# Kernel tuning notes

Measured on AMD Instinct MI355X. Metric: run time of the kernel, lower is better.

## Reference

```python
import jax, jax.numpy as jnp
import numpy as np

D_MODEL, D_INT, H = 1024, 64, 16
LAMBDA_INIT = 0.8
B, S = 2, 2048
LN_EPS = 1e-5


def setup_inputs() -> dict:
    key = jax.random.key(0)
    ks = jax.random.split(key, 12)
    sd = 0.02
    return {
        "x": jax.random.normal(ks[0], (B, S, D_MODEL), dtype=jnp.float32),
        "lambda_current": jnp.float32(0.5),
        "mask": jnp.ones((B, S), dtype=jnp.int32),
        # stacked per-head params (WQ1/WK1/WV; WQ2/WK2 are unused in source due to bug)
        "wq": sd * jax.random.normal(ks[1], (H, D_MODEL, D_INT), dtype=jnp.float32),
        "bq": sd * jax.random.normal(ks[2], (H, D_INT), dtype=jnp.float32),
        "wk": sd * jax.random.normal(ks[3], (H, D_MODEL, D_INT), dtype=jnp.float32),
        "bk": sd * jax.random.normal(ks[4], (H, D_INT), dtype=jnp.float32),
        "wv": sd * jax.random.normal(ks[5], (H, D_MODEL, 2 * D_INT), dtype=jnp.float32),
        "bv": sd * jax.random.normal(ks[6], (H, 2 * D_INT), dtype=jnp.float32),
        "wo": sd * jax.random.normal(ks[7], (2 * H * D_INT, D_MODEL), dtype=jnp.float32),
        "bo": sd * jax.random.normal(ks[8], (D_MODEL,), dtype=jnp.float32),
        "ln_g": jnp.ones((2 * D_INT,), dtype=jnp.float32),
        "ln_b": jnp.zeros((2 * D_INT,), dtype=jnp.float32),
    }


def reference(x, lambda_current, mask, wq, bq, wk, bk, wv, bv, wo, bo, ln_g, ln_b):
    b, s, d_model = x.shape
    scale = 1.0 / (d_model ** 0.5)  # source divides by sqrt(WQ1.in_features)
    # per-head projections: [H, B, S, d]
    Q = jnp.einsum('bsd,hdk->hbsk', x, wq) + bq[:, None, None, :]
    K = jnp.einsum('bsd,hdk->hbsk', x, wk) + bk[:, None, None, :]
    V = jnp.einsum('bsd,hdv->hbsv', x, wv) + bv[:, None, None, :]
    scores = jnp.einsum('hbsk,hbtk->hbst', Q, K) * scale
    scores = jnp.where(mask[None, :, None, :] == 0, -jnp.inf, scores)
    A1 = jax.nn.softmax(scores, axis=-1)
    # source bug: Q2/K2 reuse WQ1/WK1 => A2 == A1, so A = A1 - lambda*A2 = (1-lambda)*A1
    A = (1.0 - lambda_current) * A1
    out = jnp.einsum('hbst,hbtv->hbsv', A, V)  # [H,B,S,2*D_INT]
    # per-head LayerNorm (shared gamma/beta), then scale by (1 - lambda_init)
    mu = out.mean(-1, keepdims=True)
    var = out.var(-1, keepdims=True)
    out = (out - mu) / jnp.sqrt(var + LN_EPS) * ln_g + ln_b
    out = out * (1.0 - LAMBDA_INIT)
    cat = out.transpose(1, 2, 0, 3).reshape(b, s, -1)  # concat heads on feature dim
    res = cat @ wo + bo
    return (res, A)
```

## Files before the change

kernel.cpp:

```cpp
#include <hip/hip_runtime.h>
#include <hip/hip_bf16.h>

#define DM   1024
#define DI   64
#define H_   16
#define B_   2
#define S_   2048
#define NTOK 4096

typedef unsigned short u16;
typedef __attribute__((ext_vector_type(8))) short s16x8;
typedef __attribute__((ext_vector_type(4))) float f32x4;
typedef __attribute__((ext_vector_type(4))) unsigned int u32x4;
typedef __attribute__((ext_vector_type(4))) unsigned short u16x4;

static __device__ __forceinline__ u16 f2bf(float f) {
  unsigned int u = __builtin_bit_cast(unsigned int, f);
  unsigned int r = (u + 0x7fffu + ((u >> 16) & 1u)) >> 16;
  return (u16)r;
}


__global__ void k_cvt_x(const float* __restrict__ in, u16* __restrict__ out) {
  int i = (blockIdx.x * 256 + threadIdx.x) * 4;
  float4 v = *(const float4*)&in[i];
  u16x4 o;
  o[0] = f2bf(v.x); o[1] = f2bf(v.y); o[2] = f2bf(v.z); o[3] = f2bf(v.w);
  *(u16x4*)&out[i] = o;
}

__global__ void k_small(const float* __restrict__ bq, const float* __restrict__ bk,
                        const float* __restrict__ bv, const int* __restrict__ mask,
                        float* __restrict__ bc, float* __restrict__ mbias) {
  int t = blockIdx.x * 256 + threadIdx.x;
  if (t < 1024) bc[t] = bq[t];
  else if (t < 2048) bc[t] = bk[t - 1024];
  else if (t < 4096) bc[t] = bv[t - 2048];
  else if (t < 8192) { int i = t - 4096; mbias[i] = mask[i] ? 0.f : -1e38f; }
}

__global__ void k_tr_f2b(const float* __restrict__ in, u16* __restrict__ out, int R, int C) {
  __shared__ float t[32][33];
  const float* src = in + (size_t)blockIdx.z * R * C;
  u16* dst = out + (size_t)blockIdx.z * C * R;
  int r0 = blockIdx.y * 32, c0 = blockIdx.x * 32;
  for (int i = threadIdx.y; i < 32; i += 8)
    t[i][threadIdx.x] = src[(size_t)(r0 + i) * C + c0 + threadIdx.x];
  __syncthreads();
  for (int i = threadIdx.y; i < 32; i += 8)
    dst[(size_t)(c0 + i) * R + r0 + threadIdx.x] = f2bf(t[threadIdx.x][i]);
}

__global__ void k_tr_b2b(const u16* __restrict__ in, u16* __restrict__ out, int R, int C) {
  __shared__ u16 t[32][33];
  const u16* src = in + (size_t)blockIdx.z * R * C;
  u16* dst = out + (size_t)blockIdx.z * C * R;
  int r0 = blockIdx.y * 32, c0 = blockIdx.x * 32;
  for (int i = threadIdx.y; i < 32; i += 8)
    t[i][threadIdx.x] = src[(size_t)(r0 + i) * C + c0 + threadIdx.x];
  __syncthreads();
  for (int i = threadIdx.y; i < 32; i += 8)
    dst[(size_t)(c0 + i) * R + r0 + threadIdx.x] = t[threadIdx.x][i];
}

template<int MODE>
__global__ __launch_bounds__(256)
void k_gemm(const u16* __restrict__ A, const u16* __restrict__ Bt,
            const float* __restrict__ bias, int Kdim,
            u16* __restrict__ q_out, u16* __restrict__ k_out, u16* __restrict__ v_out,
            float* __restrict__ res_out) {
  const int tid = threadIdx.x;
  const int l = tid & 63, w = tid >> 6;
  const int wm = w >> 1, wn = w & 1;
  const int g = l >> 4, lo = l & 15;
  const int m0 = blockIdx.y * 128, n0 = blockIdx.x * 128;
  __shared__ u16 As[128 * 72];
  __shared__ u16 Bs[128 * 72];
  f32x4 acc[4][4] = {};
  for (int kt = 0; kt < Kdim; kt += 64) {
    __syncthreads();
    for (int cid = tid; cid < 1024; cid += 256) {
      int r = cid >> 3, c = (cid & 7) * 8;
      *(u32x4*)&As[r * 72 + c] = *(const u32x4*)&A[(size_t)(m0 + r) * Kdim + kt + c];
      *(u32x4*)&Bs[r * 72 + c] = *(const u32x4*)&Bt[(size_t)(n0 + r) * Kdim + kt + c];
    }
    __syncthreads();
    for (int kc = 0; kc < 64; kc += 32) {
      s16x8 a[4], b[4];
      for (int i = 0; i < 4; i++)
        a[i] = *(const s16x8*)&As[(wm * 64 + i * 16 + lo) * 72 + kc + 8 * g];
      for (int i = 0; i < 4; i++)
        b[i] = *(const s16x8*)&Bs[(wn * 64 + i * 16 + lo) * 72 + kc + 8 * g];
      for (int mi = 0; mi < 4; mi++)
        for (int ni = 0; ni < 4; ni++)
          acc[mi][ni] = __builtin_amdgcn_mfma_f32_16x16x32_bf16(a[mi], b[ni], acc[mi][ni], 0, 0, 0);
    }
  }
  for (int mi = 0; mi < 4; mi++)
    for (int ni = 0; ni < 4; ni++)
      for (int j = 0; j < 4; j++) {
        int m = m0 + wm * 64 + mi * 16 + g * 4 + j;
        int n = n0 + wn * 64 + ni * 16 + lo;
        float v = acc[mi][ni][j] + bias[n];
        if (MODE == 0) {
          int bb = m >> 11, s = m & 2047;
          if (n < 1024) {
            int h = n >> 6, d = n & 63;
            q_out[(((size_t)h * B_ + bb) * S_ + s) * 64 + d] = f2bf(v);
          } else if (n < 2048) {
            int nn = n - 1024; int h = nn >> 6, d = nn & 63;
            k_out[(((size_t)h * B_ + bb) * S_ + s) * 64 + d] = f2bf(v);
          } else {
            int nn = n - 2048; int h = nn >> 7, d = nn & 127;
            v_out[(((size_t)h * B_ + bb) * S_ + s) * 128 + d] = f2bf(v);
          }
        } else {
          res_out[(size_t)m * 1024 + n] = v;
        }
      }
}

__global__ __launch_bounds__(512)
void k_attn(const u16* __restrict__ Qb, const u16* __restrict__ Kb,
            const u16* __restrict__ Vtb, const float* __restrict__ mbias,
            const float* __restrict__ lam_p, const float* __restrict__ ln_g,
            const float* __restrict__ ln_b, float* __restrict__ A_out,
            u16* __restrict__ cat) {
  const int tid = threadIdx.x, l = tid & 63, w = tid >> 6;
  const int g = l >> 4, lo = l & 15;
  const int bid = blockIdx.x;
  const int xcd = bid & 7, idx = bid >> 3;
  const int hb = xcd * 4 + (idx >> 4);
  const int s0 = (idx & 15) * 128;
  const int b = hb & 1, h = hb >> 1;
  const float scale2 = 0.03125f * 1.44269504f;

  __shared__ u16 Ks[2][64 * 72];
  __shared__ u16 Vs[2][128 * 72];
  __shared__ u16 Ps[8][16 * 72];

  const u16* Qhb = Qb + (size_t)hb * S_ * 64;
  const u16* Khb = Kb + (size_t)hb * S_ * 64;
  const u16* Vthb = Vtb + (size_t)hb * 128 * S_;
  const float* mb = mbias + (size_t)b * S_;

  const int kr = tid >> 3, kc8 = (tid & 7) * 8;

  const int q = s0 + w * 16 + lo;
  const s16x8 q0 = *(const s16x8*)&Qhb[(size_t)q * 64 + 8 * g];
  const s16x8 q1 = *(const s16x8*)&Qhb[(size_t)q * 64 + 32 + 8 * g];

  {
    u32x4 kreg = *(const u32x4*)&Khb[(size_t)kr * 64 + kc8];
    *(u32x4*)&Ks[0][kr * 72 + kc8] = kreg;
  }
  __syncthreads();
  float ps = 0.f;
  for (int t = 0; t < 32; t++) {
    const int kt = t * 64, buf = t & 1;
    const int ktn = (kt + 64) & (S_ - 1);
    u32x4 kreg = *(const u32x4*)&Khb[(size_t)(ktn + kr) * 64 + kc8];
#pragma unroll
    for (int nf = 0; nf < 4; nf++) {
      s16x8 k0 = *(const s16x8*)&Ks[buf][(nf * 16 + lo) * 72 + 8 * g];
      s16x8 k1 = *(const s16x8*)&Ks[buf][(nf * 16 + lo) * 72 + 32 + 8 * g];
      f32x4 z = {};
      z = __builtin_amdgcn_mfma_f32_16x16x32_bf16(k0, q0, z, 0, 0, 0);
      z = __builtin_amdgcn_mfma_f32_16x16x32_bf16(k1, q1, z, 0, 0, 0);
      f32x4 m4 = *(const f32x4*)&mb[kt + nf * 16 + g * 4];
      ps += __builtin_exp2f(z[0] * scale2 + m4[0]);
      ps += __builtin_exp2f(z[1] * scale2 + m4[1]);
      ps += __builtin_exp2f(z[2] * scale2 + m4[2]);
      ps += __builtin_exp2f(z[3] * scale2 + m4[3]);
    }
    *(u32x4*)&Ks[buf ^ 1][kr * 72 + kc8] = kreg;
    __syncthreads();
  }
  ps += __shfl_xor(ps, 16, 64);
  ps += __shfl_xor(ps, 32, 64);
  const float rinv = (1.0f - lam_p[0]) / ps;

  {
    u32x4 v0 = *(const u32x4*)&Vthb[(size_t)(tid >> 2) * S_ + ((tid & 3) * 8 + 0)];
  }
  {
#pragma unroll
    for (int i = 0; i < 2; i++) {
      int c2 = tid + i * 512;
      int r = c2 >> 3, ch = (c2 & 7) * 8;
      *(u32x4*)&Vs[0][r * 72 + ch] = *(const u32x4*)&Vthb[(size_t)r * S_ + ch];
    }
  }
  __syncthreads();

  f32x4 o[8] = {};
  for (int t = 0; t < 32; t++) {
    const int kt = t * 64, buf = t & 1;
    u32x4 kreg;
    u32x4 vreg0, vreg1;
    const bool pre = (t < 31);
    if (pre) {
      const int ktn = kt + 64;
      kreg = *(const u32x4*)&Khb[(size_t)(ktn + kr) * 64 + kc8];
      int c2a = tid, c2b = tid + 512;
      vreg0 = *(const u32x4*)&Vthb[(size_t)(c2a >> 3) * S_ + ktn + (c2a & 7) * 8];
      vreg1 = *(const u32x4*)&Vthb[(size_t)(c2b >> 3) * S_ + ktn + (c2b & 7) * 8];
    }
#pragma unroll
    for (int nf = 0; nf < 4; nf++) {
      s16x8 k0 = *(const s16x8*)&Ks[buf][(nf * 16 + lo) * 72 + 8 * g];
      s16x8 k1 = *(const s16x8*)&Ks[buf][(nf * 16 + lo) * 72 + 32 + 8 * g];
      f32x4 z = {};
      z = __builtin_amdgcn_mfma_f32_16x16x32_bf16(k0, q0, z, 0, 0, 0);
      z = __builtin_amdgcn_mfma_f32_16x16x32_bf16(k1, q1, z, 0, 0, 0);
      f32x4 m4 = *(const f32x4*)&mb[kt + nf * 16 + g * 4];
      f32x4 p4;
      p4[0] = __builtin_exp2f(z[0] * scale2 + m4[0]) * rinv;
      p4[1] = __builtin_exp2f(z[1] * scale2 + m4[1]) * rinv;
      p4[2] = __builtin_exp2f(z[2] * scale2 + m4[2]) * rinv;
      p4[3] = __builtin_exp2f(z[3] * scale2 + m4[3]) * rinv;
      __builtin_nontemporal_store(
          p4, (f32x4*)&A_out[((size_t)hb * S_ + q) * S_ + kt + nf * 16 + g * 4]);
      u16x4 pb;
      pb[0] = f2bf(p4[0]); pb[1] = f2bf(p4[1]);
      pb[2] = f2bf(p4[2]); pb[3] = f2bf(p4[3]);
      *(u16x4*)&Ps[w][lo * 72 + nf * 16 + g * 4] = pb;
    }
#pragma unroll
    for (int kc = 0; kc < 2; kc++) {
      s16x8 pa = *(const s16x8*)&Ps[w][lo * 72 + kc * 32 + 8 * g];
#pragma unroll
      for (int vf = 0; vf < 8; vf++) {
        s16x8 bv = *(const s16x8*)&Vs[buf][(vf * 16 + lo) * 72 + kc * 32 + 8 * g];
        o[vf] = __builtin_amdgcn_mfma_f32_16x16x32_bf16(pa, bv, o[vf], 0, 0, 0);
      }
    }
    if (pre) {
      *(u32x4*)&Ks[buf ^ 1][kr * 72 + kc8] = kreg;
      int c2a = tid, c2b = tid + 512;
      *(u32x4*)&Vs[buf ^ 1][(c2a >> 3) * 72 + (c2a & 7) * 8] = vreg0;
      *(u32x4*)&Vs[buf ^ 1][(c2b >> 3) * 72 + (c2b & 7) * 8] = vreg1;
    }
    __syncthreads();
  }

#pragma unroll
  for (int j = 0; j < 4; j++) {
    float sum = 0.f, sq = 0.f;
#pragma unroll
    for (int vf = 0; vf < 8; vf++) { float xv = o[vf][j]; sum += xv; sq += xv * xv; }
    for (int msk = 1; msk < 16; msk <<= 1) {
      sum += __shfl_xor(sum, msk, 64);
      sq += __shfl_xor(sq, msk, 64);
    }
    float mean = sum * (1.f / 128.f);
    float var = sq * (1.f / 128.f) - mean * mean;
    float rstd = rsqrtf(var + 1e-5f);
    int s = s0 + w * 16 + g * 4 + j;
    u16* cp = cat + ((size_t)(b * S_ + s)) * 2048 + h * 128;
#pragma unroll
    for (int vf = 0; vf < 8; vf++) {
      int c = vf * 16 + lo;
      float y = (o[vf][j] - mean) * rstd * ln_g[c] + ln_b[c];
      cp[c] = f2bf(y * 0.2f);
    }
  }
}


extern "C" void kernel_launch(void* const* d_in, const int* in_sizes, int n_in,
                              void* d_out, int out_size, void* d_ws, size_t ws_size,
                              hipStream_t stream) {
  const float* x    = (const float*)d_in[0];
  const float* lam  = (const float*)d_in[1];
  const int*   mask = (const int*)d_in[2];
  const float* wq   = (const float*)d_in[3];
  const float* bq   = (const float*)d_in[4];
  const float* wk   = (const float*)d_in[5];
  const float* bk   = (const float*)d_in[6];
  const float* wv   = (const float*)d_in[7];
  const float* bv   = (const float*)d_in[8];
  const float* wo   = (const float*)d_in[9];
  const float* bo   = (const float*)d_in[10];
  const float* lng  = (const float*)d_in[11];
  const float* lnb  = (const float*)d_in[12];

  float* res = (float*)d_out;
  float* A   = res + (size_t)NTOK * DM;

  char* ws = (char*)d_ws;
  size_t off = 0;
  auto alloc = [&](size_t bytes) {
    void* p = ws + off;
    off += (bytes + 255) & ~(size_t)255;
    return p;
  };
  u16*   xb    = (u16*)  alloc((size_t)NTOK * DM * 2);
  u16*   Wct   = (u16*)  alloc((size_t)4096 * 1024 * 2);
  float* bc    = (float*)alloc(4096 * 4);
  float* mbias = (float*)alloc(4096 * 4);
  u16*   wot   = (u16*)  alloc((size_t)1024 * 2048 * 2);
  u16*   Qb    = (u16*)  alloc((size_t)32 * S_ * 64 * 2);
  u16*   Kb2   = (u16*)  alloc((size_t)32 * S_ * 64 * 2);
  u16*   Vb    = (u16*)  alloc((size_t)32 * S_ * 128 * 2);
  u16*   Vtb   = (u16*)  alloc((size_t)32 * S_ * 128 * 2);
  u16*   catb  = (u16*)ws;

  k_cvt_x<<<4096, 256, 0, stream>>>(x, xb);
  k_small<<<32, 256, 0, stream>>>(bq, bk, bv, mask, bc, mbias);
  k_tr_f2b<<<dim3(2, 32, 16), dim3(32, 8), 0, stream>>>(wq, Wct, 1024, 64);
  k_tr_f2b<<<dim3(2, 32, 16), dim3(32, 8), 0, stream>>>(wk, Wct + 1024 * 1024, 1024, 64);
  k_tr_f2b<<<dim3(4, 32, 16), dim3(32, 8), 0, stream>>>(wv, Wct + 2048 * 1024, 1024, 128);
  k_tr_f2b<<<dim3(32, 64, 1), dim3(32, 8), 0, stream>>>(wo, wot, 2048, 1024);
  k_gemm<0><<<dim3(32, 32), 256, 0, stream>>>(xb, Wct, bc, 1024, Qb, Kb2, Vb, nullptr);
  k_tr_b2b<<<dim3(4, 64, 32), dim3(32, 8), 0, stream>>>(Vb, Vtb, 2048, 128);
  k_attn<<<dim3(512), 512, 0, stream>>>(Qb, Kb2, Vtb, mbias, lam, lng, lnb, A, catb);
  k_gemm<1><<<dim3(8, 32), 256, 0, stream>>>(catb, wot, bo, 2048, nullptr, nullptr, nullptr, res);
}
```

Measured before the change: 400.3 us.

## Process two query tiles per attention wave and use direct global-to-LDS loads in GEMM

The attention kernel now runs 4 waves of 256 threads, each owning 32 query rows split into two 16-row halves. Each K and V fragment read from LDS is reused for twice as many MFMAs, while staging loads per thread double. Separately, the GEMM replaces register-staged LDS fills with global_load_lds 16-byte direct loads into an unpadded 64-wide tile. That layout may add LDS bank conflicts on the fragment reads, and the attention kernel uses more registers with fewer waves per block.

```diff
diff --git a/kernel.cpp b/kernel.cpp
--- a/kernel.cpp
+++ b/kernel.cpp
@@ -9,15 +9,24 @@
 #define NTOK 4096
 
 typedef unsigned short u16;
+typedef unsigned int u32;
 typedef __attribute__((ext_vector_type(8))) short s16x8;
 typedef __attribute__((ext_vector_type(4))) float f32x4;
 typedef __attribute__((ext_vector_type(4))) unsigned int u32x4;
 typedef __attribute__((ext_vector_type(4))) unsigned short u16x4;
 
+#define AS1 __attribute__((address_space(1)))
+#define AS3 __attribute__((address_space(3)))
+
 static __device__ __forceinline__ u16 f2bf(float f) {
   unsigned int u = __builtin_bit_cast(unsigned int, f);
   unsigned int r = (u + 0x7fffu + ((u >> 16) & 1u)) >> 16;
   return (u16)r;
+}
+
+static __device__ __forceinline__ void gload_lds16(const u16* g, u16* l) {
+  __builtin_amdgcn_global_load_lds((const AS1 u32*)(const void*)g,
+                                   (AS3 u32*)(void*)l, 16, 0, 0);
 }
 
 
@@ -74,23 +83,23 @@
   const int wm = w >> 1, wn = w & 1;
   const int g = l >> 4, lo = l & 15;
   const int m0 = blockIdx.y * 128, n0 = blockIdx.x * 128;
-  __shared__ u16 As[128 * 72];
-  __shared__ u16 Bs[128 * 72];
+  __shared__ u16 As[128 * 64];
+  __shared__ u16 Bs[128 * 64];
   f32x4 acc[4][4] = {};
   for (int kt = 0; kt < Kdim; kt += 64) {
     __syncthreads();
     for (int cid = tid; cid < 1024; cid += 256) {
       int r = cid >> 3, c = (cid & 7) * 8;
-      *(u32x4*)&As[r * 72 + c] = *(const u32x4*)&A[(size_t)(m0 + r) * Kdim + kt + c];
-      *(u32x4*)&Bs[r * 72 + c] = *(const u32x4*)&Bt[(size_t)(n0 + r) * Kdim + kt + c];
+      gload_lds16(&A[(size_t)(m0 + r) * Kdim + kt + c], &As[cid * 8]);
+      gload_lds16(&Bt[(size_t)(n0 + r) * Kdim + kt + c], &Bs[cid * 8]);
     }
     __syncthreads();
     for (int kc = 0; kc < 64; kc += 32) {
       s16x8 a[4], b[4];
       for (int i = 0; i < 4; i++)
-        a[i] = *(const s16x8*)&As[(wm * 64 + i * 16 + lo) * 72 + kc + 8 * g];
+        a[i] = *(const s16x8*)&As[(wm * 64 + i * 16 + lo) * 64 + kc + 8 * g];
       for (int i = 0; i < 4; i++)
-        b[i] = *(const s16x8*)&Bs[(wn * 64 + i * 16 + lo) * 72 + kc + 8 * g];
+        b[i] = *(const s16x8*)&Bs[(wn * 64 + i * 16 + lo) * 64 + kc + 8 * g];
       for (int mi = 0; mi < 4; mi++)
         for (int ni = 0; ni < 4; ni++)
           acc[mi][ni] = __builtin_amdgcn_mfma_f32_16x16x32_bf16(a[mi], b[ni], acc[mi][ni], 0, 0, 0);
@@ -120,7 +129,7 @@
       }
 }
 
-__global__ __launch_bounds__(512)
+__global__ __launch_bounds__(256)
 void k_attn(const u16* __restrict__ Qb, const u16* __restrict__ Kb,
             const u16* __restrict__ Vtb, const float* __restrict__ mbias,
             const float* __restrict__ lam_p, const float* __restrict__ ln_g,
@@ -137,132 +146,174 @@
 
   __shared__ u16 Ks[2][64 * 72];
   __shared__ u16 Vs[2][128 * 72];
-  __shared__ u16 Ps[8][16 * 72];
+  __shared__ u16 Ps[4][32 * 72];
 
   const u16* Qhb = Qb + (size_t)hb * S_ * 64;
   const u16* Khb = Kb + (size_t)hb * S_ * 64;
   const u16* Vthb = Vtb + (size_t)hb * 128 * S_;
   const float* mb = mbias + (size_t)b * S_;
 
-  const int kr = tid >> 3, kc8 = (tid & 7) * 8;
-
-  const int q = s0 + w * 16 + lo;
-  const s16x8 q0 = *(const s16x8*)&Qhb[(size_t)q * 64 + 8 * g];
-  const s16x8 q1 = *(const s16x8*)&Qhb[(size_t)q * 64 + 32 + 8 * g];
+  s16x8 q0[2], q1[2];
+#pragma unroll
+  for (int qh = 0; qh < 2; qh++) {
+    const int q = s0 + w * 32 + qh * 16 + lo;
+    q0[qh] = *(const s16x8*)&Qhb[(size_t)q * 64 + 8 * g];
+    q1[qh] = *(const s16x8*)&Qhb[(size_t)q * 64 + 32 + 8 * g];
+  }
 
   {
-    u32x4 kreg = *(const u32x4*)&Khb[(size_t)kr * 64 + kc8];
-    *(u32x4*)&Ks[0][kr * 72 + kc8] = kreg;
+#pragma unroll
+    for (int i = 0; i < 2; i++) {
+      int cid = tid + i * 256;
+      int r = cid >> 3, c = (cid & 7) * 8;
+      *(u32x4*)&Ks[0][r * 72 + c] = *(const u32x4*)&Khb[(size_t)r * 64 + c];
+    }
   }
   __syncthreads();
-  float ps = 0.f;
+  float ps[2] = {0.f, 0.f};
   for (int t = 0; t < 32; t++) {
     const int kt = t * 64, buf = t & 1;
     const int ktn = (kt + 64) & (S_ - 1);
-    u32x4 kreg = *(const u32x4*)&Khb[(size_t)(ktn + kr) * 64 + kc8];
+    u32x4 kreg[2];
+#pragma unroll
+    for (int i = 0; i < 2; i++) {
+      int cid = tid + i * 256;
+      kreg[i] = *(const u32x4*)&Khb[(size_t)(ktn + (cid >> 3)) * 64 + (cid & 7) * 8];
+    }
 #pragma unroll
     for (int nf = 0; nf < 4; nf++) {
       s16x8 k0 = *(const s16x8*)&Ks[buf][(nf * 16 + lo) * 72 + 8 * g];
       s16x8 k1 = *(const s16x8*)&Ks[buf][(nf * 16 + lo) * 72 + 32 + 8 * g];
-      f32x4 z = {};
-      z = __builtin_amdgcn_mfma_f32_16x16x32_bf16(k0, q0, z, 0, 0, 0);
-      z = __builtin_amdgcn_mfma_f32_16x16x32_bf16(k1, q1, z, 0, 0, 0);
       f32x4 m4 = *(const f32x4*)&mb[kt + nf * 16 + g * 4];
-      ps += __builtin_exp2f(z[0] * scale2 + m4[0]);
-      ps += __builtin_exp2f(z[1] * scale2 + m4[1]);
-      ps += __builtin_exp2f(z[2] * scale2 + m4[2]);
-      ps += __builtin_exp2f(z[3] * scale2 + m4[3]);
-    }
-    *(u32x4*)&Ks[buf ^ 1][kr * 72 + kc8] = kreg;
+#pragma unroll
+      for (int qh = 0; qh < 2; qh++) {
+        f32x4 z = {};
+        z = __builtin_amdgcn_mfma_f32_16x16x32_bf16(k0, q0[qh], z, 0, 0, 0);
+        z = __builtin_amdgcn_mfma_f32_16x16x32_bf16(k1, q1[qh], z, 0, 0, 0);
+        ps[qh] += __builtin_exp2f(z[0] * scale2 + m4[0]);
+        ps[qh] += __builtin_exp2f(z[1] * scale2 + m4[1]);
+        ps[qh] += __builtin_exp2f(z[2] * scale2 + m4[2]);
+        ps[qh] += __builtin_exp2f(z[3] * scale2 + m4[3]);
+      }
+    }
+#pragma unroll
+    for (int i = 0; i < 2; i++) {
+      int cid = tid + i * 256;
+      *(u32x4*)&Ks[buf ^ 1][(cid >> 3) * 72 + (cid & 7) * 8] = kreg[i];
+    }
     __syncthreads();
   }
-  ps += __shfl_xor(ps, 16, 64);
-  ps += __shfl_xor(ps, 32, 64);
-  const float rinv = (1.0f - lam_p[0]) / ps;
+  float rinv[2];
+#pragma unroll
+  for (int qh = 0; qh < 2; qh++) {
+    ps[qh] += __shfl_xor(ps[qh], 16, 64);
+    ps[qh] += __shfl_xor(ps[qh], 32, 64);
+    rinv[qh] = (1.0f - lam_p[0]) / ps[qh];
+  }
 
   {
-    u32x4 v0 = *(const u32x4*)&Vthb[(size_t)(tid >> 2) * S_ + ((tid & 3) * 8 + 0)];
-  }
-  {
-#pragma unroll
-    for (int i = 0; i < 2; i++) {
-      int c2 = tid + i * 512;
-      int r = c2 >> 3, ch = (c2 & 7) * 8;
-      *(u32x4*)&Vs[0][r * 72 + ch] = *(const u32x4*)&Vthb[(size_t)r * S_ + ch];
+#pragma unroll
+    for (int i = 0; i < 4; i++) {
+      int cid = tid + i * 256;
+      int r = cid >> 3, c = (cid & 7) * 8;
+      *(u32x4*)&Vs[0][r * 72 + c] = *(const u32x4*)&Vthb[(size_t)r * S_ + c];
     }
   }
   __syncthreads();
 
-  f32x4 o[8] = {};
+  f32x4 o[8][2] = {};
   for (int t = 0; t < 32; t++) {
     const int kt = t * 64, buf = t & 1;
-    u32x4 kreg;
-    u32x4 vreg0, vreg1;
+    u32x4 kreg[2], vreg[4];
     const bool pre = (t < 31);
     if (pre) {
       const int ktn = kt + 64;
-      kreg = *(const u32x4*)&Khb[(size_t)(ktn + kr) * 64 + kc8];
-      int c2a = tid, c2b = tid + 512;
-      vreg0 = *(const u32x4*)&Vthb[(size_t)(c2a >> 3) * S_ + ktn + (c2a & 7) * 8];
-      vreg1 = *(const u32x4*)&Vthb[(size_t)(c2b >> 3) * S_ + ktn + (c2b & 7) * 8];
+#pragma unroll
+      for (int i = 0; i < 2; i++) {
+        int cid = tid + i * 256;
+        kreg[i] = *(const u32x4*)&Khb[(size_t)(ktn + (cid >> 3)) * 64 + (cid & 7) * 8];
+      }
+#pragma unroll
+      for (int i = 0; i < 4; i++) {
+        int cid = tid + i * 256;
+        vreg[i] = *(const u32x4*)&Vthb[(size_t)(cid >> 3) * S_ + ktn + (cid & 7) * 8];
+      }
     }
 #pragma unroll
     for (int nf = 0; nf < 4; nf++) {
       s16x8 k0 = *(const s16x8*)&Ks[buf][(nf * 16 + lo) * 72 + 8 * g];
       s16x8 k1 = *(const s16x8*)&Ks[buf][(nf * 16 + lo) * 72 + 32 + 8 * g];
-      f32x4 z = {};
-      z = __builtin_amdgcn_mfma_f32_16x16x32_bf16(k0, q0, z, 0, 0, 0);
-      z = __builtin_amdgcn_mfma_f32_16x16x32_bf16(k1, q1, z, 0, 0, 0);
       f32x4 m4 = *(const f32x4*)&mb[kt + nf * 16 + g * 4];
-      f32x4 p4;
-      p4[0] = __builtin_exp2f(z[0] * scale2 + m4[0]) * rinv;
-      p4[1] = __builtin_exp2f(z[1] * scale2 + m4[1]) * rinv;
-      p4[2] = __builtin_exp2f(z[2] * scale2 + m4[2]) * rinv;
-      p4[3] = __builtin_exp2f(z[3] * scale2 + m4[3]) * rinv;
-      __builtin_nontemporal_store(
-          p4, (f32x4*)&A_out[((size_t)hb * S_ + q) * S_ + kt + nf * 16 + g * 4]);
-      u16x4 pb;
-      pb[0] = f2bf(p4[0]); pb[1] = f2bf(p4[1]);
-      pb[2] = f2bf(p4[2]); pb[3] = f2bf(p4[3]);
-      *(u16x4*)&Ps[w][lo * 72 + nf * 16 + g * 4] = pb;
+#pragma unroll
+      for (int qh = 0; qh < 2; qh++) {
+        f32x4 z = {};
+        z = __builtin_amdgcn_mfma_f32_16x16x32_bf16(k0, q0[qh], z, 0, 0, 0);
+        z = __builtin_amdgcn_mfma_f32_16x16x32_bf16(k1, q1[qh], z, 0, 0, 0);
+        f32x4 p4;
+        p4[0] = __builtin_exp2f(z[0] * scale2 + m4[0]) * rinv[qh];
+        p4[1] = __builtin_exp2f(z[1] * scale2 + m4[1]) * rinv[qh];
+        p4[2] = __builtin_exp2f(z[2] * scale2 + m4[2]) * rinv[qh];
+        p4[3] = __builtin_exp2f(z[3] * scale2 + m4[3]) * rinv[qh];
+        const int q = s0 + w * 32 + qh * 16 + lo;
+        __builtin_nontemporal_store(
+            p4, (f32x4*)&A_out[((size_t)hb * S_ + q) * S_ + kt + nf * 16 + g * 4]);
+        u16x4 pb;
+        pb[0] = f2bf(p4[0]); pb[1] = f2bf(p4[1]);
+        pb[2] = f2bf(p4[2]); pb[3] = f2bf(p4[3]);
+        *(u16x4*)&Ps[w][(qh * 16 + lo) * 72 + nf * 16 + g * 4] = pb;
+      }
     }
 #pragma unroll
     for (int kc = 0; kc < 2; kc++) {
-      s16x8 pa = *(const s16x8*)&Ps[w][lo * 72 + kc * 32 + 8 * g];
+      s16x8 pa[2];
+#pragma unroll
+      for (int qh = 0; qh < 2; qh++)
+        pa[qh] = *(const s16x8*)&Ps[w][(qh * 16 + lo) * 72 + kc * 32 + 8 * g];
 #pragma unroll
       for (int vf = 0; vf < 8; vf++) {
         s16x8 bv = *(const s16x8*)&Vs[buf][(vf * 16 + lo) * 72 + kc * 32 + 8 * g];
-        o[vf] = __builtin_amdgcn_mfma_f32_16x16x32_bf16(pa, bv, o[vf], 0, 0, 0);
+#pragma unroll
+        for (int qh = 0; qh < 2; qh++)
+          o[vf][qh] = __builtin_amdgcn_mfma_f32_16x16x32_bf16(pa[qh], bv, o[vf][qh], 0, 0, 0);
       }
     }
     if (pre) {
-      *(u32x4*)&Ks[buf ^ 1][kr * 72 + kc8] = kreg;
-      int c2a = tid, c2b = tid + 512;
-      *(u32x4*)&Vs[buf ^ 1][(c2a >> 3) * 72 + (c2a & 7) * 8] = vreg0;
-      *(u32x4*)&Vs[buf ^ 1][(c2b >> 3) * 72 + (c2b & 7) * 8] = vreg1;
+#pragma unroll
+      for (int i = 0; i < 2; i++) {
+        int cid = tid + i * 256;
+        *(u32x4*)&Ks[buf ^ 1][(cid >> 3) * 72 + (cid & 7) * 8] = kreg[i];
+      }
+#pragma unroll
+      for (int i = 0; i < 4; i++) {
+        int cid = tid + i * 256;
+        *(u32x4*)&Vs[buf ^ 1][(cid >> 3) * 72 + (cid & 7) * 8] = vreg[i];
+      }
     }
     __syncthreads();
   }
 
 #pragma unroll
-  for (int j = 0; j < 4; j++) {
-    float sum = 0.f, sq = 0.f;
-#pragma unroll
-    for (int vf = 0; vf < 8; vf++) { float xv = o[vf][j]; sum += xv; sq += xv * xv; }
-    for (int msk = 1; msk < 16; msk <<= 1) {
-      sum += __shfl_xor(sum, msk, 64);
-      sq += __shfl_xor(sq, msk, 64);
-    }
-    float mean = sum * (1.f / 128.f);
-    float var = sq * (1.f / 128.f) - mean * mean;
-    float rstd = rsqrtf(var + 1e-5f);
-    int s = s0 + w * 16 + g * 4 + j;
-    u16* cp = cat + ((size_t)(b * S_ + s)) * 2048 + h * 128;
-#pragma unroll
-    for (int vf = 0; vf < 8; vf++) {
-      int c = vf * 16 + lo;
-      float y = (o[vf][j] - mean) * rstd * ln_g[c] + ln_b[c];
-      cp[c] = f2bf(y * 0.2f);
+  for (int qh = 0; qh < 2; qh++) {
+#pragma unroll
+    for (int j = 0; j < 4; j++) {
+      float sum = 0.f, sq = 0.f;
+#pragma unroll
+      for (int vf = 0; vf < 8; vf++) { float xv = o[vf][qh][j]; sum += xv; sq += xv * xv; }
+      for (int msk = 1; msk < 16; msk <<= 1) {
+        sum += __shfl_xor(sum, msk, 64);
+        sq += __shfl_xor(sq, msk, 64);
+      }
+      float mean = sum * (1.f / 128.f);
+      float var = sq * (1.f / 128.f) - mean * mean;
+      float rstd = rsqrtf(var + 1e-5f);
+      int s = s0 + w * 32 + qh * 16 + g * 4 + j;
+      u16* cp = cat + ((size_t)(b * S_ + s)) * 2048 + h * 128;
+#pragma unroll
+      for (int vf = 0; vf < 8; vf++) {
+        int c = vf * 16 + lo;
+        float y = (o[vf][qh][j] - mean) * rstd * ln_g[c] + ln_b[c];
+        cp[c] = f2bf(y * 0.2f);
+      }
     }
   }
 }
@@ -314,6 +365,6 @@
   k_tr_f2b<<<dim3(32, 64, 1), dim3(32, 8), 0, stream>>>(wo, wot, 2048, 1024);
   k_gemm<0><<<dim3(32, 32), 256, 0, stream>>>(xb, Wct, bc, 1024, Qb, Kb2, Vb, nullptr);
   k_tr_b2b<<<dim3(4, 64, 32), dim3(32, 8), 0, stream>>>(Vb, Vtb, 2048, 128);
-  k_attn<<<dim3(512), 512, 0, stream>>>(Qb, Kb2, Vtb, mbias, lam, lng, lnb, A, catb);
+  k_attn<<<dim3(512), 256, 0, stream>>>(Qb, Kb2, Vtb, mbias, lam, lng, lnb, A, catb);
   k_gemm<1><<<dim3(8, 32), 256, 0, stream>>>(catb, wot, bo, 2048, nullptr, nullptr, nullptr, res);
 }
```

After: 372.2 us. 7.0% less time.

## Shrink attention blocks to 256 threads, single-buffer LDS, direct global-to-LDS GEMM loads

Applied to the files above, without the earlier changes.

The attention kernel now uses 64-query blocks of 256 threads (1024 blocks) with single-buffered K/V LDS tiles, launch bounds for 4 blocks per CU, and an extra barrier per tile to split QK from PV. The first pass reuses the V buffer as the second K buffer. The GEMM swaps register-staged tile loads for global_load_lds into unpadded LDS. The aim is higher occupancy and less LDS per block. The cost is more barriers, twice the K/V reloads across blocks, and possible LDS bank conflicts from the unpadded GEMM layout.

```diff
diff --git a/kernel.cpp b/kernel.cpp
--- a/kernel.cpp
+++ b/kernel.cpp
@@ -9,15 +9,24 @@
 #define NTOK 4096
 
 typedef unsigned short u16;
+typedef unsigned int u32;
 typedef __attribute__((ext_vector_type(8))) short s16x8;
 typedef __attribute__((ext_vector_type(4))) float f32x4;
 typedef __attribute__((ext_vector_type(4))) unsigned int u32x4;
 typedef __attribute__((ext_vector_type(4))) unsigned short u16x4;
 
+#define AS1 __attribute__((address_space(1)))
+#define AS3 __attribute__((address_space(3)))
+
 static __device__ __forceinline__ u16 f2bf(float f) {
   unsigned int u = __builtin_bit_cast(unsigned int, f);
   unsigned int r = (u + 0x7fffu + ((u >> 16) & 1u)) >> 16;
   return (u16)r;
+}
+
+static __device__ __forceinline__ void gload_lds16(const u16* g, u16* l) {
+  __builtin_amdgcn_global_load_lds((const AS1 u32*)(const void*)g,
+                                   (AS3 u32*)(void*)l, 16, 0, 0);
 }
 
 
@@ -74,23 +83,23 @@
   const int wm = w >> 1, wn = w & 1;
   const int g = l >> 4, lo = l & 15;
   const int m0 = blockIdx.y * 128, n0 = blockIdx.x * 128;
-  __shared__ u16 As[128 * 72];
-  __shared__ u16 Bs[128 * 72];
+  __shared__ u16 As[128 * 64];
+  __shared__ u16 Bs[128 * 64];
   f32x4 acc[4][4] = {};
   for (int kt = 0; kt < Kdim; kt += 64) {
     __syncthreads();
     for (int cid = tid; cid < 1024; cid += 256) {
       int r = cid >> 3, c = (cid & 7) * 8;
-      *(u32x4*)&As[r * 72 + c] = *(const u32x4*)&A[(size_t)(m0 + r) * Kdim + kt + c];
-      *(u32x4*)&Bs[r * 72 + c] = *(const u32x4*)&Bt[(size_t)(n0 + r) * Kdim + kt + c];
+      gload_lds16(&A[(size_t)(m0 + r) * Kdim + kt + c], &As[cid * 8]);
+      gload_lds16(&Bt[(size_t)(n0 + r) * Kdim + kt + c], &Bs[cid * 8]);
     }
     __syncthreads();
     for (int kc = 0; kc < 64; kc += 32) {
       s16x8 a[4], b[4];
       for (int i = 0; i < 4; i++)
-        a[i] = *(const s16x8*)&As[(wm * 64 + i * 16 + lo) * 72 + kc + 8 * g];
+        a[i] = *(const s16x8*)&As[(wm * 64 + i * 16 + lo) * 64 + kc + 8 * g];
       for (int i = 0; i < 4; i++)
-        b[i] = *(const s16x8*)&Bs[(wn * 64 + i * 16 + lo) * 72 + kc + 8 * g];
+        b[i] = *(const s16x8*)&Bs[(wn * 64 + i * 16 + lo) * 64 + kc + 8 * g];
       for (int mi = 0; mi < 4; mi++)
         for (int ni = 0; ni < 4; ni++)
           acc[mi][ni] = __builtin_amdgcn_mfma_f32_16x16x32_bf16(a[mi], b[ni], acc[mi][ni], 0, 0, 0);
@@ -120,7 +129,7 @@
       }
 }
 
-__global__ __launch_bounds__(512)
+__global__ __launch_bounds__(256, 4)
 void k_attn(const u16* __restrict__ Qb, const u16* __restrict__ Kb,
             const u16* __restrict__ Vtb, const float* __restrict__ mbias,
             const float* __restrict__ lam_p, const float* __restrict__ ln_g,
@@ -130,97 +139,110 @@
   const int g = l >> 4, lo = l & 15;
   const int bid = blockIdx.x;
   const int xcd = bid & 7, idx = bid >> 3;
-  const int hb = xcd * 4 + (idx >> 4);
-  const int s0 = (idx & 15) * 128;
+  const int hb = xcd * 4 + (idx >> 5);
+  const int s0 = (idx & 31) * 64;
   const int b = hb & 1, h = hb >> 1;
   const float scale2 = 0.03125f * 1.44269504f;
-
-  __shared__ u16 Ks[2][64 * 72];
-  __shared__ u16 Vs[2][128 * 72];
-  __shared__ u16 Ps[8][16 * 72];
+  const float pfac = 1.0f - lam_p[0];
+
+  __shared__ __align__(16) u16 Ks[64 * 72];
+  __shared__ __align__(16) u16 Vs[128 * 72];
+  __shared__ __align__(16) u16 Ps[4][16 * 72];
 
   const u16* Qhb = Qb + (size_t)hb * S_ * 64;
   const u16* Khb = Kb + (size_t)hb * S_ * 64;
   const u16* Vthb = Vtb + (size_t)hb * 128 * S_;
   const float* mb = mbias + (size_t)b * S_;
 
-  const int kr = tid >> 3, kc8 = (tid & 7) * 8;
-
   const int q = s0 + w * 16 + lo;
   const s16x8 q0 = *(const s16x8*)&Qhb[(size_t)q * 64 + 8 * g];
   const s16x8 q1 = *(const s16x8*)&Qhb[(size_t)q * 64 + 32 + 8 * g];
+  float* Arow = A_out + ((size_t)hb * S_ + q) * S_;
+
+  const int kr = tid >> 3, kc8 = (tid & 7) * 8;
 
   {
-    u32x4 kreg = *(const u32x4*)&Khb[(size_t)kr * 64 + kc8];
-    *(u32x4*)&Ks[0][kr * 72 + kc8] = kreg;
+    *(u32x4*)&Ks[kr * 72 + kc8] = *(const u32x4*)&Khb[(size_t)kr * 64 + kc8];
+    int cid = tid + 256; int r = cid >> 3, c = (cid & 7) * 8;
+    *(u32x4*)&Ks[r * 72 + c] = *(const u32x4*)&Khb[(size_t)r * 64 + c];
   }
   __syncthreads();
-  float ps = 0.f;
+  f32x4 psv = {};
   for (int t = 0; t < 32; t++) {
-    const int kt = t * 64, buf = t & 1;
+    const u16* rbuf = (t & 1) ? Vs : Ks;
+    u16* wbuf = (t & 1) ? Ks : Vs;
+    const int kt = t * 64;
     const int ktn = (kt + 64) & (S_ - 1);
-    u32x4 kreg = *(const u32x4*)&Khb[(size_t)(ktn + kr) * 64 + kc8];
+    u32x4 kreg0 = *(const u32x4*)&Khb[(size_t)(ktn + kr) * 64 + kc8];
+    u32x4 kreg1 = *(const u32x4*)&Khb[(size_t)(ktn + kr + 32) * 64 + kc8];
 #pragma unroll
     for (int nf = 0; nf < 4; nf++) {
-      s16x8 k0 = *(const s16x8*)&Ks[buf][(nf * 16 + lo) * 72 + 8 * g];
-      s16x8 k1 = *(const s16x8*)&Ks[buf][(nf * 16 + lo) * 72 + 32 + 8 * g];
+      s16x8 k0 = *(const s16x8*)&rbuf[(nf * 16 + lo) * 72 + 8 * g];
+      s16x8 k1 = *(const s16x8*)&rbuf[(nf * 16 + lo) * 72 + 32 + 8 * g];
       f32x4 z = {};
       z = __builtin_amdgcn_mfma_f32_16x16x32_bf16(k0, q0, z, 0, 0, 0);
       z = __builtin_amdgcn_mfma_f32_16x16x32_bf16(k1, q1, z, 0, 0, 0);
       f32x4 m4 = *(const f32x4*)&mb[kt + nf * 16 + g * 4];
-      ps += __builtin_exp2f(z[0] * scale2 + m4[0]);
-      ps += __builtin_exp2f(z[1] * scale2 + m4[1]);
-      ps += __builtin_exp2f(z[2] * scale2 + m4[2]);
-      ps += __builtin_exp2f(z[3] * scale2 + m4[3]);
-    }
-    *(u32x4*)&Ks[buf ^ 1][kr * 72 + kc8] = kreg;
-    __syncthreads();
-  }
+      psv[0] += __builtin_exp2f(z[0] * scale2 + m4[0]);
+      psv[1] += __builtin_exp2f(z[1] * scale2 + m4[1]);
+      psv[2] += __builtin_exp2f(z[2] * scale2 + m4[2]);
+      psv[3] += __builtin_exp2f(z[3] * scale2 + m4[3]);
+    }
+    *(u32x4*)&wbuf[kr * 72 + kc8] = kreg0;
+    *(u32x4*)&wbuf[(kr + 32) * 72 + kc8] = kreg1;
+    __syncthreads();
+  }
+  float ps = (psv[0] + psv[1]) + (psv[2] + psv[3]);
   ps += __shfl_xor(ps, 16, 64);
   ps += __shfl_xor(ps, 32, 64);
-  const float rinv = (1.0f - lam_p[0]) / ps;
-
-  {
-    u32x4 v0 = *(const u32x4*)&Vthb[(size_t)(tid >> 2) * S_ + ((tid & 3) * 8 + 0)];
-  }
-  {
-#pragma unroll
-    for (int i = 0; i < 2; i++) {
-      int c2 = tid + i * 512;
-      int r = c2 >> 3, ch = (c2 & 7) * 8;
-      *(u32x4*)&Vs[0][r * 72 + ch] = *(const u32x4*)&Vthb[(size_t)r * S_ + ch];
-    }
+  const float rinv = pfac / ps;
+
+#pragma unroll
+  for (int i = 0; i < 4; i++) {
+    int cid = tid + i * 256;
+    int r = cid >> 3, c = (cid & 7) * 8;
+    *(u32x4*)&Vs[r * 72 + c] = *(const u32x4*)&Vthb[(size_t)r * S_ + c];
   }
   __syncthreads();
 
   f32x4 o[8] = {};
   for (int t = 0; t < 32; t++) {
-    const int kt = t * 64, buf = t & 1;
-    u32x4 kreg;
-    u32x4 vreg0, vreg1;
+    const int kt = t * 64;
     const bool pre = (t < 31);
+    u32x4 kreg0, kreg1, vreg[4];
     if (pre) {
       const int ktn = kt + 64;
-      kreg = *(const u32x4*)&Khb[(size_t)(ktn + kr) * 64 + kc8];
-      int c2a = tid, c2b = tid + 512;
-      vreg0 = *(const u32x4*)&Vthb[(size_t)(c2a >> 3) * S_ + ktn + (c2a & 7) * 8];
-      vreg1 = *(const u32x4*)&Vthb[(size_t)(c2b >> 3) * S_ + ktn + (c2b & 7) * 8];
-    }
+      kreg0 = *(const u32x4*)&Khb[(size_t)(ktn + kr) * 64 + kc8];
+      kreg1 = *(const u32x4*)&Khb[(size_t)(ktn + kr + 32) * 64 + kc8];
+#pragma unroll
+      for (int i = 0; i < 4; i++) {
+        int cid = tid + i * 256;
+        vreg[i] = *(const u32x4*)&Vthb[(size_t)(cid >> 3) * S_ + ktn + (cid & 7) * 8];
+      }
+    }
+    f32x4 z[4];
 #pragma unroll
     for (int nf = 0; nf < 4; nf++) {
-      s16x8 k0 = *(const s16x8*)&Ks[buf][(nf * 16 + lo) * 72 + 8 * g];
-      s16x8 k1 = *(const s16x8*)&Ks[buf][(nf * 16 + lo) * 72 + 32 + 8 * g];
-      f32x4 z = {};
-      z = __builtin_amdgcn_mfma_f32_16x16x32_bf16(k0, q0, z, 0, 0, 0);
-      z = __builtin_amdgcn_mfma_f32_16x16x32_bf16(k1, q1, z, 0, 0, 0);
+      s16x8 k0 = *(const s16x8*)&Ks[(nf * 16 + lo) * 72 + 8 * g];
+      s16x8 k1 = *(const s16x8*)&Ks[(nf * 16 + lo) * 72 + 32 + 8 * g];
+      f32x4 zz = {};
+      zz = __builtin_amdgcn_mfma_f32_16x16x32_bf16(k0, q0, zz, 0, 0, 0);
+      z[nf] = __builtin_amdgcn_mfma_f32_16x16x32_bf16(k1, q1, zz, 0, 0, 0);
+    }
+    __syncthreads();
+    if (pre) {
+      *(u32x4*)&Ks[kr * 72 + kc8] = kreg0;
+      *(u32x4*)&Ks[(kr + 32) * 72 + kc8] = kreg1;
+    }
+#pragma unroll
+    for (int nf = 0; nf < 4; nf++) {
       f32x4 m4 = *(const f32x4*)&mb[kt + nf * 16 + g * 4];
       f32x4 p4;
-      p4[0] = __builtin_exp2f(z[0] * scale2 + m4[0]) * rinv;
-      p4[1] = __builtin_exp2f(z[1] * scale2 + m4[1]) * rinv;
-      p4[2] = __builtin_exp2f(z[2] * scale2 + m4[2]) * rinv;
-      p4[3] = __builtin_exp2f(z[3] * scale2 + m4[3]) * rinv;
-      __builtin_nontemporal_store(
-          p4, (f32x4*)&A_out[((size_t)hb * S_ + q) * S_ + kt + nf * 16 + g * 4]);
+      p4[0] = __builtin_exp2f(z[nf][0] * scale2 + m4[0]) * rinv;
+      p4[1] = __builtin_exp2f(z[nf][1] * scale2 + m4[1]) * rinv;
+      p4[2] = __builtin_exp2f(z[nf][2] * scale2 + m4[2]) * rinv;
+      p4[3] = __builtin_exp2f(z[nf][3] * scale2 + m4[3]) * rinv;
+      __builtin_nontemporal_store(p4, (f32x4*)&Arow[kt + nf * 16 + g * 4]);
       u16x4 pb;
       pb[0] = f2bf(p4[0]); pb[1] = f2bf(p4[1]);
       pb[2] = f2bf(p4[2]); pb[3] = f2bf(p4[3]);
@@ -231,17 +253,18 @@
       s16x8 pa = *(const s16x8*)&Ps[w][lo * 72 + kc * 32 + 8 * g];
 #pragma unroll
       for (int vf = 0; vf < 8; vf++) {
-        s16x8 bv = *(const s16x8*)&Vs[buf][(vf * 16 + lo) * 72 + kc * 32 + 8 * g];
+        s16x8 bv = *(const s16x8*)&Vs[(vf * 16 + lo) * 72 + kc * 32 + 8 * g];
         o[vf] = __builtin_amdgcn_mfma_f32_16x16x32_bf16(pa, bv, o[vf], 0, 0, 0);
       }
     }
+    __syncthreads();
     if (pre) {
-      *(u32x4*)&Ks[buf ^ 1][kr * 72 + kc8] = kreg;
-      int c2a = tid, c2b = tid + 512;
-      *(u32x4*)&Vs[buf ^ 1][(c2a >> 3) * 72 + (c2a & 7) * 8] = vreg0;
-      *(u32x4*)&Vs[buf ^ 1][(c2b >> 3) * 72 + (c2b & 7) * 8] = vreg1;
-    }
-    __syncthreads();
+#pragma unroll
+      for (int i = 0; i < 4; i++) {
+        int cid = tid + i * 256;
+        *(u32x4*)&Vs[(cid >> 3) * 72 + (cid & 7) * 8] = vreg[i];
+      }
+    }
   }
 
 #pragma unroll
@@ -314,6 +337,6 @@
   k_tr_f2b<<<dim3(32, 64, 1), dim3(32, 8), 0, stream>>>(wo, wot, 2048, 1024);
   k_gemm<0><<<dim3(32, 32), 256, 0, stream>>>(xb, Wct, bc, 1024, Qb, Kb2, Vb, nullptr);
   k_tr_b2b<<<dim3(4, 64, 32), dim3(32, 8), 0, stream>>>(Vb, Vtb, 2048, 128);
-  k_attn<<<dim3(512), 512, 0, stream>>>(Qb, Kb2, Vtb, mbias, lam, lng, lnb, A, catb);
+  k_attn<<<dim3(1024), 256, 0, stream>>>(Qb, Kb2, Vtb, mbias, lam, lng, lnb, A, catb);
   k_gemm<1><<<dim3(8, 32), 256, 0, stream>>>(catb, wot, bo, 2048, nullptr, nullptr, nullptr, res);
 }
```

Result: faster. 358.9 us (-10.3%).
